# Optimization experiments

Hardware: AMD Instinct MI355X
Metric: run time of the kernel (lower is better)

Reference implementation:

```python
import jax, jax.numpy as jnp
import numpy as np

HIDDEN_DIM = 2048
NUM_CONN = int(HIDDEN_DIM * HIDDEN_DIM * 0.1)  # 419430


def setup_inputs() -> dict:
    key = jax.random.key(0)
    k1, k2, k3 = jax.random.split(key, 3)
    x = jax.random.normal(k1, (4, 2048, HIDDEN_DIM), dtype=jnp.float32)
    connection_indices = jax.random.randint(k2, (2, NUM_CONN), 0, HIDDEN_DIM, dtype=jnp.int64)
    connection_values = jax.random.normal(k3, (NUM_CONN,), dtype=jnp.float32) * 0.001
    alpha = jnp.asarray(0.01, dtype=jnp.float32)
    return {"x": x, "connection_indices": connection_indices,
            "connection_values": connection_values, "alpha": alpha}


def reference(x, connection_indices, connection_values, alpha):
    # Rebuild dense W from COO (duplicate indices sum, matching sparse_coo_tensor.to_dense())
    H = x.shape[-1]
    W = jnp.zeros((H, H), dtype=x.dtype).at[connection_indices[0], connection_indices[1]].add(connection_values)
    # torch.matmul(x, W.T): out[b,s,i] = sum_j x[b,s,j] * W[i,j]
    lateral = jnp.einsum('bsj,ij->bsi', x, W)
    return x + alpha * lateral
```

## Files before the change

### kernel.cpp

```cpp
#include <hip/hip_runtime.h>


typedef unsigned short u16;
typedef __attribute__((ext_vector_type(8))) short bf16x8;
typedef __attribute__((ext_vector_type(4))) float f32x4;

#define HID 2048
#define BM 256
#define BN 256
#define BK 32
#define NT (HID / BK)
#define SLOT_ELEMS (BM * BK + BN * BK)
#define HALF_ELEMS (128 * BK)

__device__ __forceinline__ u16 f2bf(float f) {
    unsigned u = __builtin_bit_cast(unsigned, f);
    u += 0x7fffu + ((u >> 16) & 1u);
    return (u16)(u >> 16);
}

__device__ __forceinline__ void cvt8(const float* __restrict__ src,
                                     u16* __restrict__ dst, int i) {
    const float4* p = (const float4*)src + (size_t)i * 2;
    float4 a = p[0], b = p[1];
    uint4 o;
    o.x = (unsigned)f2bf(a.x) | ((unsigned)f2bf(a.y) << 16);
    o.y = (unsigned)f2bf(a.z) | ((unsigned)f2bf(a.w) << 16);
    o.z = (unsigned)f2bf(b.x) | ((unsigned)f2bf(b.y) << 16);
    o.w = (unsigned)f2bf(b.z) | ((unsigned)f2bf(b.w) << 16);
    ((uint4*)dst)[i] = o;
}

__global__ void cvt_f32_bf16_kernel(const float* __restrict__ in,
                                    u16* __restrict__ out, int n8) {
    int stride = gridDim.x * blockDim.x;
    for (int i = blockIdx.x * blockDim.x + threadIdx.x; i < n8; i += stride)
        cvt8(in, out, i);
}

__global__ void cvt_both_kernel(const float* __restrict__ w,
                                const float* __restrict__ x,
                                u16* __restrict__ wb, u16* __restrict__ xb,
                                int n8w, int n8x) {
    int stride = gridDim.x * blockDim.x;
    int total = n8w + n8x;
    for (int i = blockIdx.x * blockDim.x + threadIdx.x; i < total; i += stride) {
        if (i < n8w) cvt8(w, wb, i);
        else         cvt8(x, xb, i - n8w);
    }
}

__global__ void scatter_coo_kernel(const int* __restrict__ idx,
                                   const float* __restrict__ vals,
                                   float* __restrict__ W, int nnz) {
    int n = blockIdx.x * blockDim.x + threadIdx.x;
    if (n < nnz) {
        int i = idx[n];
        int j = idx[nnz + n];
        atomicAdd(W + (size_t)i * HID + j, vals[n]);
    }
}

#define GLDS(gsrc, ldst)                                                   \
    __builtin_amdgcn_global_load_lds(                                      \
        (const __attribute__((address_space(1))) void*)(gsrc),             \
        (__attribute__((address_space(3))) void*)(ldst), 16, 0, 0)

__global__ __launch_bounds__(512, 2) void gemm8_kernel(
        const u16* __restrict__ A,
        const u16* __restrict__ B,
        const float* __restrict__ Xf,
        const float* __restrict__ alphap,
        float* __restrict__ out) {
    __shared__ u16 lds[4 * SLOT_ELEMS];

    const int t = threadIdx.x;
    const int lane = t & 63;
    const int w = t >> 6;
    const int wr = w >> 2;
    const int wc = w & 3;
    const int fr = lane & 15;
    const int kg = lane >> 4;

    const int bid = blockIdx.x;
    const int swz = (bid & 7) * 32 + (bid >> 3);
    const int bm = swz >> 3;
    const int bn = swz & 7;
    const size_t rowBase = (size_t)bm * BM;
    const size_t colBase = (size_t)bn * BN;

    const int srow = (w << 4) + (lane >> 2);
    const int sg = (lane & 3) ^ ((srow >> 1) & 3);
    const u16* aSrc = A + (rowBase + srow) * HID + sg * 8;
    const u16* bSrc = B + (colBase + srow) * HID + sg * 8;
    const int ldst = (w << 9) + (lane << 3);

    const int gread = kg ^ ((fr >> 1) & 3);

    f32x4 acc[8][4] = {};

    for (int pt = 0; pt < 3; ++pt) {
        u16* slot = lds + (pt & 3) * SLOT_ELEMS;
        const u16* as = aSrc + pt * BK;
        const u16* bs = bSrc + pt * BK;
        GLDS(as,             slot + ldst);
        GLDS(bs,             slot + 2 * HALF_ELEMS + ldst);
        GLDS(as + 128 * HID, slot + HALF_ELEMS + ldst);
        GLDS(bs + 128 * HID, slot + 3 * HALF_ELEMS + ldst);
    }
    asm volatile("s_waitcnt vmcnt(8)" ::: "memory");
    __builtin_amdgcn_s_barrier();
    __builtin_amdgcn_sched_barrier(0);

#pragma unroll 1
    for (int tt = 0; tt < NT; ++tt) {
        u16* slot  = lds + (tt & 3) * SLOT_ELEMS;
        u16* slot3 = lds + ((tt + 3) & 3) * SLOT_ELEMS;
        const int t3 = tt + 3;
        const u16* as3 = aSrc + t3 * BK;
        const u16* bs3 = bSrc + t3 * BK;
        const u16* aRd = slot + (wr * 128 + fr) * BK + gread * 8;
        const u16* bRd = slot + 2 * HALF_ELEMS + (wc * 64 + fr) * BK + gread * 8;

        bf16x8 b[4];

        bf16x8 a0[4];
#pragma unroll
        for (int m = 0; m < 4; ++m)
            a0[m] = *(const bf16x8*)(aRd + m * 16 * BK);
#pragma unroll
        for (int n = 0; n < 4; ++n)
            b[n] = *(const bf16x8*)(bRd + n * 16 * BK);
        if (t3 < NT) {
            GLDS(as3, slot3 + ldst);
            GLDS(bs3, slot3 + 2 * HALF_ELEMS + ldst);
        }
        asm volatile("s_waitcnt lgkmcnt(0)" ::: "memory");
        __builtin_amdgcn_s_barrier();
        __builtin_amdgcn_sched_barrier(0);
        __builtin_amdgcn_s_setprio(1);
#pragma unroll
        for (int m = 0; m < 4; ++m)
#pragma unroll
            for (int n = 0; n < 4; ++n)
                acc[m][n] = __builtin_amdgcn_mfma_f32_16x16x32_bf16(
                    a0[m], b[n], acc[m][n], 0, 0, 0);
        __builtin_amdgcn_s_setprio(0);

        bf16x8 a1[4];
#pragma unroll
        for (int m = 0; m < 4; ++m)
            a1[m] = *(const bf16x8*)(aRd + (m + 4) * 16 * BK);
        if (t3 < NT) {
            GLDS(as3 + 128 * HID, slot3 + HALF_ELEMS + ldst);
            GLDS(bs3 + 128 * HID, slot3 + 3 * HALF_ELEMS + ldst);
        }
        asm volatile("s_waitcnt lgkmcnt(0)" ::: "memory");
        if (tt < NT - 3)       asm volatile("s_waitcnt vmcnt(8)" ::: "memory");
        else if (tt == NT - 3) asm volatile("s_waitcnt vmcnt(4)" ::: "memory");
        else if (tt == NT - 2) asm volatile("s_waitcnt vmcnt(0)" ::: "memory");
        __builtin_amdgcn_s_barrier();
        __builtin_amdgcn_sched_barrier(0);
        __builtin_amdgcn_s_setprio(1);
#pragma unroll
        for (int m = 0; m < 4; ++m)
#pragma unroll
            for (int n = 0; n < 4; ++n)
                acc[m + 4][n] = __builtin_amdgcn_mfma_f32_16x16x32_bf16(
                    a1[m], b[n], acc[m + 4][n], 0, 0, 0);
        __builtin_amdgcn_s_setprio(0);
    }

    const float alphav = *alphap;
#pragma unroll
    for (int m = 0; m < 8; ++m) {
#pragma unroll
        for (int n = 0; n < 4; ++n) {
            f32x4 c = acc[m][n];
            const size_t gn = colBase + wc * 64 + n * 16 + fr;
#pragma unroll
            for (int j = 0; j < 4; ++j) {
                const size_t gm = rowBase + wr * 128 + m * 16 + kg * 4 + j;
                const size_t o = gm * HID + gn;
                out[o] = Xf[o] + alphav * c[j];
            }
        }
    }
}

extern "C" void kernel_launch(void* const* d_in, const int* in_sizes, int n_in,
                              void* d_out, int out_size, void* d_ws, size_t ws_size,
                              hipStream_t stream) {
    const float* x     = (const float*)d_in[0];
    const int*   idx   = (const int*)d_in[1];
    const float* vals  = (const float*)d_in[2];
    const float* alpha = (const float*)d_in[3];
    float* out = (float*)d_out;

    const int nnz = in_sizes[2];
    const size_t MB = 1024 * 1024;
    const int n8W = (HID * HID) / 8;
    const int n8X = in_sizes[0] / 8;

    if (ws_size >= 56 * MB) {
        u16*   Xb = (u16*)d_ws;
        u16*   Wb = (u16*)((char*)d_ws + 32 * MB);
        float* Wf = (float*)((char*)d_ws + 40 * MB);
        hipMemsetAsync(Wf, 0, (size_t)HID * HID * sizeof(float), stream);
        scatter_coo_kernel<<<(nnz + 255) / 256, 256, 0, stream>>>(idx, vals, Wf, nnz);
        cvt_both_kernel<<<2048, 256, 0, stream>>>(Wf, x, Wb, Xb, n8W, n8X);
        gemm8_kernel<<<256, 512, 0, stream>>>(Xb, Wb, x, alpha, out);
    } else {
        float* Wf = (float*)d_ws;
        u16*   Xb = (u16*)d_ws;
        u16*   Wb = (u16*)((char*)d_ws + 32 * MB);
        hipMemsetAsync(Wf, 0, (size_t)HID * HID * sizeof(float), stream);
        scatter_coo_kernel<<<(nnz + 255) / 256, 256, 0, stream>>>(idx, vals, Wf, nnz);
        cvt_f32_bf16_kernel<<<2048, 256, 0, stream>>>(Wf, Wb, n8W);
        cvt_f32_bf16_kernel<<<2048, 256, 0, stream>>>(x, Xb, n8X);
        gemm8_kernel<<<256, 512, 0, stream>>>(Xb, Wb, x, alpha, out);
    }
}
```

Before: 212.0 us.

## Retile GEMM to 128x256 with 3-stage pipeline, fuse prep, read bf16 residual

Shrinks the GEMM block tile from 256x256 to 128x256 and launches 512 blocks. It switches from a 4-slot to a 3-slot LDS ring, which cuts shared memory per block and allows more resident blocks per CU. It fuses the COO scatter with the x fp32-to-bf16 conversion into one prep kernel. The epilogue now reads the residual x from the bf16 copy instead of fp32 and uses nontemporal stores. This halves epilogue read traffic, but the residual add loses precision because x is rounded to bf16.

```diff
diff --git a/kernel.cpp b/kernel.cpp
--- a/kernel.cpp
+++ b/kernel.cpp
@@ -6,12 +6,13 @@
 typedef __attribute__((ext_vector_type(4))) float f32x4;
 
 #define HID 2048
-#define BM 256
+#define BM 128
 #define BN 256
 #define BK 32
 #define NT (HID / BK)
-#define SLOT_ELEMS (BM * BK + BN * BK)
-#define HALF_ELEMS (128 * BK)
+#define ASZ (BM * BK)
+#define BSZ (BN * BK)
+#define SLOT (ASZ + BSZ)
 
 __device__ __forceinline__ u16 f2bf(float f) {
     unsigned u = __builtin_bit_cast(unsigned, f);
@@ -38,27 +39,25 @@
         cvt8(in, out, i);
 }
 
-__global__ void cvt_both_kernel(const float* __restrict__ w,
-                                const float* __restrict__ x,
-                                u16* __restrict__ wb, u16* __restrict__ xb,
-                                int n8w, int n8x) {
-    int stride = gridDim.x * blockDim.x;
-    int total = n8w + n8x;
-    for (int i = blockIdx.x * blockDim.x + threadIdx.x; i < total; i += stride) {
-        if (i < n8w) cvt8(w, wb, i);
-        else         cvt8(x, xb, i - n8w);
-    }
-}
-
 __global__ void scatter_coo_kernel(const int* __restrict__ idx,
                                    const float* __restrict__ vals,
                                    float* __restrict__ W, int nnz) {
     int n = blockIdx.x * blockDim.x + threadIdx.x;
-    if (n < nnz) {
-        int i = idx[n];
-        int j = idx[nnz + n];
-        atomicAdd(W + (size_t)i * HID + j, vals[n]);
-    }
+    if (n < nnz)
+        atomicAdd(W + (size_t)idx[n] * HID + idx[nnz + n], vals[n]);
+}
+
+__global__ void prep_kernel(const int* __restrict__ idx,
+                            const float* __restrict__ vals,
+                            float* __restrict__ W, int nnz,
+                            const float* __restrict__ x,
+                            u16* __restrict__ xb, int n8x) {
+    int gid = blockIdx.x * blockDim.x + threadIdx.x;
+    if (gid < nnz)
+        atomicAdd(W + (size_t)idx[gid] * HID + idx[nnz + gid], vals[gid]);
+    int stride = gridDim.x * blockDim.x;
+    for (int i = gid; i < n8x; i += stride)
+        cvt8(x, xb, i);
 }
 
 #define GLDS(gsrc, ldst)                                                   \
@@ -66,13 +65,12 @@
         (const __attribute__((address_space(1))) void*)(gsrc),             \
         (__attribute__((address_space(3))) void*)(ldst), 16, 0, 0)
 
-__global__ __launch_bounds__(512, 2) void gemm8_kernel(
+__global__ __launch_bounds__(512, 4) void gemm3_kernel(
         const u16* __restrict__ A,
         const u16* __restrict__ B,
-        const float* __restrict__ Xf,
         const float* __restrict__ alphap,
         float* __restrict__ out) {
-    __shared__ u16 lds[4 * SLOT_ELEMS];
+    __shared__ u16 lds[3 * SLOT];
 
     const int t = threadIdx.x;
     const int lane = t & 63;
@@ -83,106 +81,96 @@
     const int kg = lane >> 4;
 
     const int bid = blockIdx.x;
-    const int swz = (bid & 7) * 32 + (bid >> 3);
+    const int swz = (bid & 7) * 64 + (bid >> 3);
     const int bm = swz >> 3;
     const int bn = swz & 7;
     const size_t rowBase = (size_t)bm * BM;
     const size_t colBase = (size_t)bn * BN;
 
-    const int srow = (w << 4) + (lane >> 2);
-    const int sg = (lane & 3) ^ ((srow >> 1) & 3);
-    const u16* aSrc = A + (rowBase + srow) * HID + sg * 8;
-    const u16* bSrc = B + (colBase + srow) * HID + sg * 8;
-    const int ldst = (w << 9) + (lane << 3);
+    const int srowA = (w << 4) + (lane >> 2);
+    const int sgA = (lane & 3) ^ ((srowA >> 1) & 3);
+    const u16* aSrc = A + (rowBase + srowA) * HID + sgA * 8;
+    const int adst = w * 512 + lane * 8;
+
+    const int srowB = (w << 5) + (lane >> 2);
+    const int sgB = (lane & 3) ^ ((srowB >> 1) & 3);
+    const u16* bSrc0 = B + (colBase + srowB) * HID + sgB * 8;
+    const u16* bSrc1 = bSrc0 + (size_t)16 * HID;
+    const int bdst0 = ASZ + w * 1024 + lane * 8;
+    const int bdst1 = bdst0 + 512;
 
     const int gread = kg ^ ((fr >> 1) & 3);
-
-    f32x4 acc[8][4] = {};
-
-    for (int pt = 0; pt < 3; ++pt) {
-        u16* slot = lds + (pt & 3) * SLOT_ELEMS;
-        const u16* as = aSrc + pt * BK;
-        const u16* bs = bSrc + pt * BK;
-        GLDS(as,             slot + ldst);
-        GLDS(bs,             slot + 2 * HALF_ELEMS + ldst);
-        GLDS(as + 128 * HID, slot + HALF_ELEMS + ldst);
-        GLDS(bs + 128 * HID, slot + 3 * HALF_ELEMS + ldst);
-    }
-    asm volatile("s_waitcnt vmcnt(8)" ::: "memory");
+    const int aRdOff = (wr * 64 + fr) * BK + gread * 8;
+    const int bRdOff = ASZ + (wc * 64 + fr) * BK + gread * 8;
+
+    f32x4 acc[4][4] = {};
+
+#pragma unroll
+    for (int pt = 0; pt < 2; ++pt) {
+        u16* s = lds + pt * SLOT;
+        GLDS(aSrc + pt * BK, s + adst);
+        GLDS(bSrc0 + pt * BK, s + bdst0);
+        GLDS(bSrc1 + pt * BK, s + bdst1);
+    }
+    asm volatile("s_waitcnt vmcnt(3)" ::: "memory");
     __builtin_amdgcn_s_barrier();
     __builtin_amdgcn_sched_barrier(0);
 
+    int cur = 0;
 #pragma unroll 1
     for (int tt = 0; tt < NT; ++tt) {
-        u16* slot  = lds + (tt & 3) * SLOT_ELEMS;
-        u16* slot3 = lds + ((tt + 3) & 3) * SLOT_ELEMS;
-        const int t3 = tt + 3;
-        const u16* as3 = aSrc + t3 * BK;
-        const u16* bs3 = bSrc + t3 * BK;
-        const u16* aRd = slot + (wr * 128 + fr) * BK + gread * 8;
-        const u16* bRd = slot + 2 * HALF_ELEMS + (wc * 64 + fr) * BK + gread * 8;
-
-        bf16x8 b[4];
-
-        bf16x8 a0[4];
+        u16* slot = lds + cur * SLOT;
+        const int wIdx = cur + 2 >= 3 ? cur - 1 : cur + 2;
+        u16* slotW = lds + wIdx * SLOT;
+
+        bf16x8 a[4], b[4];
 #pragma unroll
         for (int m = 0; m < 4; ++m)
-            a0[m] = *(const bf16x8*)(aRd + m * 16 * BK);
+            a[m] = *(const bf16x8*)(slot + aRdOff + m * 512);
 #pragma unroll
         for (int n = 0; n < 4; ++n)
-            b[n] = *(const bf16x8*)(bRd + n * 16 * BK);
-        if (t3 < NT) {
-            GLDS(as3, slot3 + ldst);
-            GLDS(bs3, slot3 + 2 * HALF_ELEMS + ldst);
+            b[n] = *(const bf16x8*)(slot + bRdOff + n * 512);
+
+        if (tt + 2 < NT) {
+            const int koff = (tt + 2) * BK;
+            GLDS(aSrc + koff, slotW + adst);
+            GLDS(bSrc0 + koff, slotW + bdst0);
+            GLDS(bSrc1 + koff, slotW + bdst1);
         }
+
         asm volatile("s_waitcnt lgkmcnt(0)" ::: "memory");
-        __builtin_amdgcn_s_barrier();
         __builtin_amdgcn_sched_barrier(0);
-        __builtin_amdgcn_s_setprio(1);
-#pragma unroll
-        for (int m = 0; m < 4; ++m)
-#pragma unroll
-            for (int n = 0; n < 4; ++n)
-                acc[m][n] = __builtin_amdgcn_mfma_f32_16x16x32_bf16(
-                    a0[m], b[n], acc[m][n], 0, 0, 0);
-        __builtin_amdgcn_s_setprio(0);
-
-        bf16x8 a1[4];
-#pragma unroll
-        for (int m = 0; m < 4; ++m)
-            a1[m] = *(const bf16x8*)(aRd + (m + 4) * 16 * BK);
-        if (t3 < NT) {
-            GLDS(as3 + 128 * HID, slot3 + HALF_ELEMS + ldst);
-            GLDS(bs3 + 128 * HID, slot3 + 3 * HALF_ELEMS + ldst);
-        }
-        asm volatile("s_waitcnt lgkmcnt(0)" ::: "memory");
-        if (tt < NT - 3)       asm volatile("s_waitcnt vmcnt(8)" ::: "memory");
-        else if (tt == NT - 3) asm volatile("s_waitcnt vmcnt(4)" ::: "memory");
+        if (tt <= NT - 3)      asm volatile("s_waitcnt vmcnt(3)" ::: "memory");
         else if (tt == NT - 2) asm volatile("s_waitcnt vmcnt(0)" ::: "memory");
         __builtin_amdgcn_s_barrier();
         __builtin_amdgcn_sched_barrier(0);
+
         __builtin_amdgcn_s_setprio(1);
 #pragma unroll
         for (int m = 0; m < 4; ++m)
 #pragma unroll
             for (int n = 0; n < 4; ++n)
-                acc[m + 4][n] = __builtin_amdgcn_mfma_f32_16x16x32_bf16(
-                    a1[m], b[n], acc[m + 4][n], 0, 0, 0);
+                acc[m][n] = __builtin_amdgcn_mfma_f32_16x16x32_bf16(
+                    a[m], b[n], acc[m][n], 0, 0, 0);
         __builtin_amdgcn_s_setprio(0);
+
+        cur = cur == 2 ? 0 : cur + 1;
     }
 
     const float alphav = *alphap;
 #pragma unroll
-    for (int m = 0; m < 8; ++m) {
+    for (int m = 0; m < 4; ++m) {
 #pragma unroll
         for (int n = 0; n < 4; ++n) {
             f32x4 c = acc[m][n];
             const size_t gn = colBase + wc * 64 + n * 16 + fr;
 #pragma unroll
             for (int j = 0; j < 4; ++j) {
-                const size_t gm = rowBase + wr * 128 + m * 16 + kg * 4 + j;
+                const size_t gm = rowBase + wr * 64 + m * 16 + kg * 4 + j;
                 const size_t o = gm * HID + gn;
-                out[o] = Xf[o] + alphav * c[j];
+                unsigned xu = ((unsigned)A[o]) << 16;
+                float xf = __builtin_bit_cast(float, xu);
+                __builtin_nontemporal_store(xf + alphav * c[j], &out[o]);
             }
         }
     }
@@ -201,15 +189,16 @@
     const size_t MB = 1024 * 1024;
     const int n8W = (HID * HID) / 8;
     const int n8X = in_sizes[0] / 8;
+    const int grid = (8192 / BM) * (HID / BN);
 
     if (ws_size >= 56 * MB) {
         u16*   Xb = (u16*)d_ws;
         u16*   Wb = (u16*)((char*)d_ws + 32 * MB);
         float* Wf = (float*)((char*)d_ws + 40 * MB);
         hipMemsetAsync(Wf, 0, (size_t)HID * HID * sizeof(float), stream);
-        scatter_coo_kernel<<<(nnz + 255) / 256, 256, 0, stream>>>(idx, vals, Wf, nnz);
-        cvt_both_kernel<<<2048, 256, 0, stream>>>(Wf, x, Wb, Xb, n8W, n8X);
-        gemm8_kernel<<<256, 512, 0, stream>>>(Xb, Wb, x, alpha, out);
+        prep_kernel<<<2048, 256, 0, stream>>>(idx, vals, Wf, nnz, x, Xb, n8X);
+        cvt_f32_bf16_kernel<<<2048, 256, 0, stream>>>(Wf, Wb, n8W);
+        gemm3_kernel<<<grid, 512, 0, stream>>>(Xb, Wb, alpha, out);
     } else {
         float* Wf = (float*)d_ws;
         u16*   Xb = (u16*)d_ws;
@@ -218,6 +207,6 @@
         scatter_coo_kernel<<<(nnz + 255) / 256, 256, 0, stream>>>(idx, vals, Wf, nnz);
         cvt_f32_bf16_kernel<<<2048, 256, 0, stream>>>(Wf, Wb, n8W);
         cvt_f32_bf16_kernel<<<2048, 256, 0, stream>>>(x, Xb, n8X);
-        gemm8_kernel<<<256, 512, 0, stream>>>(Xb, Wb, x, alpha, out);
-    }
-}
+        gemm3_kernel<<<grid, 512, 0, stream>>>(Xb, Wb, alpha, out);
+    }
+}
```

Measured after the change: 211.4 us. No clear change (-0.3%).
